# Optimization experiments

Hardware: AMD Instinct MI355X
Metric: run time of the kernel (lower is better)

## Reference

```python
import jax, jax.numpy as jnp
import numpy as np

N_NODES = 50000
N_EDGES = 800000
D_IN = 64
D_HID = 64
N_LAYERS = 3
BN_EPS = 1e-5


def setup_inputs() -> dict:
    key = jax.random.key(0)
    ks = jax.random.split(key, 10)
    x = jax.random.normal(ks[0], (N_NODES, D_IN), dtype=jnp.float32)
    edge_index = jax.random.randint(ks[1], (2, N_EDGES), 0, N_NODES, dtype=jnp.int32)
    # Per-layer GCN weights (in==hid==64 so we can stack) and BatchNorm params.
    Ws = jax.random.normal(ks[2], (N_LAYERS, D_HID, D_HID), dtype=jnp.float32) / np.sqrt(D_HID)
    bs = jnp.zeros((N_LAYERS, D_HID), dtype=jnp.float32)
    gammas = jnp.ones((N_LAYERS, D_HID), dtype=jnp.float32)
    betas = jnp.zeros((N_LAYERS, D_HID), dtype=jnp.float32)
    means = jax.random.normal(ks[3], (N_LAYERS, D_HID), dtype=jnp.float32) * 0.1
    variances = jax.random.uniform(ks[4], (N_LAYERS, D_HID), dtype=jnp.float32, minval=0.5, maxval=1.5)
    lin_w = jax.random.normal(ks[5], (D_HID, 1), dtype=jnp.float32) / np.sqrt(D_HID)
    lin_b = jnp.zeros((1,), dtype=jnp.float32)
    return {"x": x, "edge_index": edge_index, "Ws": Ws, "bs": bs,
            "gammas": gammas, "betas": betas, "means": means,
            "variances": variances, "lin_w": lin_w, "lin_b": lin_b}


def _gnn_forward(x, edge_index, Ws, bs, gammas, betas, means, variances, lin_w, lin_b):
    n = x.shape[0]
    # GCNConv: add self loops, symmetric D^{-1/2}(A+I)D^{-1/2} normalization.
    loop = jnp.arange(n, dtype=edge_index.dtype)
    row = jnp.concatenate([edge_index[0], loop])  # source nodes
    col = jnp.concatenate([edge_index[1], loop])  # target nodes
    deg = jax.ops.segment_sum(jnp.ones(row.shape[0], x.dtype), col, num_segments=n)
    dinv = jax.lax.rsqrt(jnp.maximum(deg, 1.0))  # deg >= 1 from self loops
    norm = (dinv[row] * dinv[col])[:, None]  # [E+N, 1]

    h = x
    for i in range(N_LAYERS):
        h = h @ Ws[i]  # transform first (PyG GCNConv order)
        h = jax.ops.segment_sum(h[row] * norm, col, num_segments=n) + bs[i]
        # BatchNorm1d (eval mode: running stats) + ReLU; dropout is identity in eval.
        h = (h - means[i]) * jax.lax.rsqrt(variances[i] + BN_EPS) * gammas[i] + betas[i]
        h = jax.nn.relu(h)
    out = h @ lin_w + lin_b  # [N, 1]
    return out[:, 0]


def reference(x, edge_index, Ws, bs, gammas, betas, means, variances, lin_w, lin_b):
    return _gnn_forward(x, edge_index, Ws, bs, gammas, betas, means, variances, lin_w, lin_b)
```

## Files before the change

### kernel.cpp

```cpp
#include <hip/hip_runtime.h>
#include <hip/hip_bf16.h>


#define BN_EPS 1e-5f
#define CAP 64
#define CHUNK 4096
#define SEGCAP 5120
#define NBINS_MAX 256

__global__ __launch_bounds__(256) void k_bin_pairs(const int* __restrict__ row,
                                                   const int* __restrict__ col,
                                                   int* __restrict__ gfill,
                                                   unsigned int* __restrict__ gpairs,
                                                   int e, int nbins) {
    __shared__ unsigned int pl[CHUNK];
    __shared__ int bcnt[NBINS_MAX];
    __shared__ int bbase[NBINS_MAX];
    int tid = threadIdx.x;
    int base = blockIdx.x * CHUNK;
    for (int b = tid; b < nbins; b += 256) bcnt[b] = 0;
    __syncthreads();
    int nloc = e - base; if (nloc > CHUNK) nloc = CHUNK;
    #pragma unroll
    for (int it = 0; it < CHUNK / 1024; ++it) {
        int le = (it * 256 + tid) * 4;
        if (le + 3 < nloc) {
            int i4 = (base >> 2) + it * 256 + tid;
            int4 r = ((const int4*)row)[i4];
            int4 c = ((const int4*)col)[i4];
            atomicAdd(&bcnt[c.x >> 8], 1); pl[le + 0] = (unsigned)r.x | ((unsigned)c.x << 16);
            atomicAdd(&bcnt[c.y >> 8], 1); pl[le + 1] = (unsigned)r.y | ((unsigned)c.y << 16);
            atomicAdd(&bcnt[c.z >> 8], 1); pl[le + 2] = (unsigned)r.z | ((unsigned)c.z << 16);
            atomicAdd(&bcnt[c.w >> 8], 1); pl[le + 3] = (unsigned)r.w | ((unsigned)c.w << 16);
        } else {
            for (int j = 0; j < 4; ++j) {
                if (le + j < nloc) {
                    int rr = row[base + le + j];
                    int cc = col[base + le + j];
                    atomicAdd(&bcnt[cc >> 8], 1);
                    pl[le + j] = (unsigned)rr | ((unsigned)cc << 16);
                }
            }
        }
    }
    __syncthreads();
    for (int b = tid; b < nbins; b += 256) {
        bbase[b] = atomicAdd(&gfill[b], bcnt[b]);
        bcnt[b] = 0;
    }
    __syncthreads();
    for (int i = tid; i < nloc; i += 256) {
        unsigned int p = pl[i];
        int bin = p >> 24;
        int off = atomicAdd(&bcnt[bin], 1);
        int pos = bbase[bin] + off;
        if (pos < SEGCAP) gpairs[(size_t)bin * SEGCAP + pos] = p;
    }
}

__global__ __launch_bounds__(256) void k_bucket_build(const unsigned int* __restrict__ gpairs,
                                                      const int* __restrict__ gfill,
                                                      int* __restrict__ cnt,
                                                      unsigned short* __restrict__ bucket,
                                                      int n) {
    __shared__ unsigned short lb[256 * CAP];
    __shared__ int lc[256];
    int tid = threadIdx.x;
    int bin = blockIdx.x;
    lc[tid] = 0;
    __syncthreads();
    int m = gfill[bin]; if (m > SEGCAP) m = SEGCAP;
    const unsigned int* seg = gpairs + (size_t)bin * SEGCAP;
    for (int i = tid; i < m; i += 256) {
        unsigned int p = seg[i];
        int src = p & 0xffff;
        int dl = (p >> 16) & 255;
        int pos = atomicAdd(&lc[dl], 1);
        if (pos < CAP) lb[dl * CAP + pos] = (unsigned short)src;
    }
    __syncthreads();
    int nodebase = bin << 8;
    const int4* lb4 = (const int4*)lb;
    int4* gb4 = (int4*)bucket;
    for (int i = tid; i < 256 * 8; i += 256) {
        int rrow = i >> 3;
        int gnode = nodebase + rrow;
        if (gnode < n) gb4[(size_t)gnode * 8 + (i & 7)] = lb4[i];
    }
    int gnode = nodebase + tid;
    if (gnode < n) cnt[gnode] = lc[tid];
}

template<int LAYER>
__global__ __launch_bounds__(256) void k_matmul(const float* __restrict__ A,
                                                const float* __restrict__ W,
                                                const int* __restrict__ cnt,
                                                float* __restrict__ out, int n) {
    __shared__ float hs[64 * 65];
    __shared__ float wsh[64 * 64];
    int tid = threadIdx.x;
    int rbase = blockIdx.x * 64;
    for (int i = tid; i < 4096; i += 256) wsh[i] = W[i];
    for (int i = tid; i < 4096; i += 256) {
        int r = i >> 6, c = i & 63;
        int gr = rbase + r;
        hs[r * 65 + c] = (gr < n) ? A[gr * 64 + c] : 0.f;
    }
    __syncthreads();
    int r = tid & 63;
    int cg = tid >> 6;
    float4 a0 = {0, 0, 0, 0}, a1 = a0, a2 = a0, a3 = a0;
    const float4* W4 = (const float4*)wsh;
    #pragma unroll 8
    for (int k = 0; k < 64; ++k) {
        float hv = hs[r * 65 + k];
        float4 w0 = W4[k * 16 + cg * 4 + 0];
        float4 w1 = W4[k * 16 + cg * 4 + 1];
        float4 w2 = W4[k * 16 + cg * 4 + 2];
        float4 w3 = W4[k * 16 + cg * 4 + 3];
        a0.x = fmaf(hv, w0.x, a0.x); a0.y = fmaf(hv, w0.y, a0.y);
        a0.z = fmaf(hv, w0.z, a0.z); a0.w = fmaf(hv, w0.w, a0.w);
        a1.x = fmaf(hv, w1.x, a1.x); a1.y = fmaf(hv, w1.y, a1.y);
        a1.z = fmaf(hv, w1.z, a1.z); a1.w = fmaf(hv, w1.w, a1.w);
        a2.x = fmaf(hv, w2.x, a2.x); a2.y = fmaf(hv, w2.y, a2.y);
        a2.z = fmaf(hv, w2.z, a2.z); a2.w = fmaf(hv, w2.w, a2.w);
        a3.x = fmaf(hv, w3.x, a3.x); a3.y = fmaf(hv, w3.y, a3.y);
        a3.z = fmaf(hv, w3.z, a3.z); a3.w = fmaf(hv, w3.w, a3.w);
    }
    int gr = rbase + r;
    if (gr < n) {
        float d = rsqrtf((float)(cnt[gr] + 1));
        a0.x *= d; a0.y *= d; a0.z *= d; a0.w *= d;
        a1.x *= d; a1.y *= d; a1.z *= d; a1.w *= d;
        a2.x *= d; a2.y *= d; a2.z *= d; a2.w *= d;
        a3.x *= d; a3.y *= d; a3.z *= d; a3.w *= d;
        float4* o = (float4*)(out + gr * 64 + cg * 16);
        o[0] = a0; o[1] = a1; o[2] = a2; o[3] = a3;
    }
}

template<int LAYER, bool FINAL>
__global__ __launch_bounds__(256) void k_agg(const float* __restrict__ t,
                                             const int* __restrict__ cnt,
                                             const unsigned short* __restrict__ bucket,
                                             const float* __restrict__ bias,
                                             const float* __restrict__ gamma,
                                             const float* __restrict__ beta,
                                             const float* __restrict__ mean,
                                             const float* __restrict__ var,
                                             float* __restrict__ hout,
                                             const float* __restrict__ lw,
                                             const float* __restrict__ lb,
                                             float* __restrict__ outp, int n) {
    int node = (blockIdx.x * blockDim.x + threadIdx.x) >> 6;
    if (node >= n) return;
    int lane = threadIdx.x & 63;
    int g = lane >> 4;
    int fl = (lane & 15) << 2;
    int c = cnt[node];
    int myidx = (int)bucket[node * CAP + lane];
    float4 acc = {0.f, 0.f, 0.f, 0.f};
    int sub = 0;
    for (; sub + 8 <= c; sub += 8) {
        int sA = __shfl(myidx, sub + g, 64);
        int sB = __shfl(myidx, sub + 4 + g, 64);
        float4 vA = *(const float4*)(t + (size_t)sA * 64 + fl);
        float4 vB = *(const float4*)(t + (size_t)sB * 64 + fl);
        acc.x += vA.x; acc.y += vA.y; acc.z += vA.z; acc.w += vA.w;
        acc.x += vB.x; acc.y += vB.y; acc.z += vB.z; acc.w += vB.w;
    }
    for (; sub < c; sub += 4) {
        int j = sub + g;
        int jj = (j < c) ? j : c - 1;
        int sA = __shfl(myidx, jj, 64);
        if (j < c) {
            float4 v = *(const float4*)(t + (size_t)sA * 64 + fl);
            acc.x += v.x; acc.y += v.y; acc.z += v.z; acc.w += v.w;
        }
    }
    acc.x += __shfl_down(acc.x, 32, 64); acc.y += __shfl_down(acc.y, 32, 64);
    acc.z += __shfl_down(acc.z, 32, 64); acc.w += __shfl_down(acc.w, 32, 64);
    acc.x += __shfl_down(acc.x, 16, 64); acc.y += __shfl_down(acc.y, 16, 64);
    acc.z += __shfl_down(acc.z, 16, 64); acc.w += __shfl_down(acc.w, 16, 64);
    if (lane < 16) {
        float di = rsqrtf((float)(c + 1));
        float4 self = *(const float4*)(t + (size_t)node * 64 + fl);
        float4 b4 = *(const float4*)(bias + fl);
        float4 m4 = *(const float4*)(mean + fl);
        float4 v4 = *(const float4*)(var + fl);
        float4 g4 = *(const float4*)(gamma + fl);
        float4 be4 = *(const float4*)(beta + fl);
        float4 r;
        r.x = fmaf(acc.x + self.x, di, b4.x);
        r.y = fmaf(acc.y + self.y, di, b4.y);
        r.z = fmaf(acc.z + self.z, di, b4.z);
        r.w = fmaf(acc.w + self.w, di, b4.w);
        float4 h;
        h.x = fmaxf(fmaf(r.x - m4.x, g4.x * rsqrtf(v4.x + BN_EPS), be4.x), 0.f);
        h.y = fmaxf(fmaf(r.y - m4.y, g4.y * rsqrtf(v4.y + BN_EPS), be4.y), 0.f);
        h.z = fmaxf(fmaf(r.z - m4.z, g4.z * rsqrtf(v4.z + BN_EPS), be4.z), 0.f);
        h.w = fmaxf(fmaf(r.w - m4.w, g4.w * rsqrtf(v4.w + BN_EPS), be4.w), 0.f);
        if (FINAL) {
            float4 w4 = *(const float4*)(lw + fl);
            float p = h.x * w4.x + h.y * w4.y + h.z * w4.z + h.w * w4.w;
            p += __shfl_down(p, 8, 64);
            p += __shfl_down(p, 4, 64);
            p += __shfl_down(p, 2, 64);
            p += __shfl_down(p, 1, 64);
            if (lane == 0) outp[node] = p + lb[0];
        } else {
            *(float4*)(hout + (size_t)node * 64 + fl) = h;
        }
    }
}

extern "C" void kernel_launch(void* const* d_in, const int* in_sizes, int n_in,
                              void* d_out, int out_size, void* d_ws, size_t ws_size,
                              hipStream_t stream) {
    const float* x    = (const float*)d_in[0];
    const int*   ei   = (const int*)d_in[1];
    const float* Ws   = (const float*)d_in[2];
    const float* bs   = (const float*)d_in[3];
    const float* gam  = (const float*)d_in[4];
    const float* bet  = (const float*)d_in[5];
    const float* mean = (const float*)d_in[6];
    const float* var  = (const float*)d_in[7];
    const float* lw   = (const float*)d_in[8];
    const float* lb   = (const float*)d_in[9];
    float* out = (float*)d_out;

    const int n = in_sizes[0] / 64;
    const int e = in_sizes[1] / 2;
    const int* row = ei;
    const int* col = ei + e;
    const int nbins = (n + 255) >> 8;

    int*   ws_i = (int*)d_ws;
    float* ws_f = (float*)d_ws;
    int* cnt = ws_i;
    int* gfill = ws_i + n;
    unsigned short* bucket = (unsigned short*)(ws_i + n + 256);
    float* tbuf = ws_f + n + 256 + 32 * (size_t)n;
    float* hbuf = tbuf + 64 * (size_t)n;
    unsigned int* gpairs = (unsigned int*)tbuf;

    int nb_p1 = (e + CHUNK - 1) / CHUNK;
    int nb_w = (n + 3) / 4;
    int nb_mm = (n + 63) / 64;

    hipMemsetAsync(gfill, 0, 256 * sizeof(int), stream);
    k_bin_pairs<<<nb_p1, 256, 0, stream>>>(row, col, gfill, gpairs, e, nbins);
    k_bucket_build<<<nbins, 256, 0, stream>>>(gpairs, gfill, cnt, bucket, n);

    k_matmul<0><<<nb_mm, 256, 0, stream>>>(x, Ws + 0 * 4096, cnt, tbuf, n);
    k_agg<0, false><<<nb_w, 256, 0, stream>>>(tbuf, cnt, bucket,
                                              bs, gam, bet, mean, var,
                                              hbuf, nullptr, nullptr, nullptr, n);
    k_matmul<1><<<nb_mm, 256, 0, stream>>>(hbuf, Ws + 1 * 4096, cnt, tbuf, n);
    k_agg<1, false><<<nb_w, 256, 0, stream>>>(tbuf, cnt, bucket,
                                              bs + 64, gam + 64, bet + 64, mean + 64, var + 64,
                                              hbuf, nullptr, nullptr, nullptr, n);
    k_matmul<2><<<nb_mm, 256, 0, stream>>>(hbuf, Ws + 2 * 4096, cnt, tbuf, n);
    k_agg<2, true><<<nb_w, 256, 0, stream>>>(tbuf, cnt, bucket,
                                             bs + 128, gam + 128, bet + 128, mean + 128, var + 128,
                                             nullptr, lw, lb, out, n);
}
```

Baseline: 271.5 us.

## Fuse GCN matmul into aggregation by reordering aggregate-then-transform per layer

Uses linearity to aggregate first and multiply by W afterwards. This folds the separate matmul kernels into a single persistent per-layer kernel that keeps W columns in registers and does the 64x64 transform through wave shuffles. The input is pre-scaled by the degree normalisation once, and each layer writes its output already scaled for the next. The goal is to cut three kernel launches and a full read/write round trip of the feature matrix per layer. The cost is 64 shuffle-FMA steps per node, heavy register use from the 64-float array, and a grid fixed at 1024 blocks.

```diff
diff --git a/kernel.cpp b/kernel.cpp
--- a/kernel.cpp
+++ b/kernel.cpp
@@ -91,125 +91,102 @@
     if (gnode < n) cnt[gnode] = lc[tid];
 }
 
-template<int LAYER>
-__global__ __launch_bounds__(256) void k_matmul(const float* __restrict__ A,
-                                                const float* __restrict__ W,
-                                                const int* __restrict__ cnt,
-                                                float* __restrict__ out, int n) {
-    __shared__ float hs[64 * 65];
-    __shared__ float wsh[64 * 64];
-    int tid = threadIdx.x;
-    int rbase = blockIdx.x * 64;
-    for (int i = tid; i < 4096; i += 256) wsh[i] = W[i];
-    for (int i = tid; i < 4096; i += 256) {
-        int r = i >> 6, c = i & 63;
-        int gr = rbase + r;
-        hs[r * 65 + c] = (gr < n) ? A[gr * 64 + c] : 0.f;
-    }
-    __syncthreads();
-    int r = tid & 63;
-    int cg = tid >> 6;
-    float4 a0 = {0, 0, 0, 0}, a1 = a0, a2 = a0, a3 = a0;
-    const float4* W4 = (const float4*)wsh;
-    #pragma unroll 8
-    for (int k = 0; k < 64; ++k) {
-        float hv = hs[r * 65 + k];
-        float4 w0 = W4[k * 16 + cg * 4 + 0];
-        float4 w1 = W4[k * 16 + cg * 4 + 1];
-        float4 w2 = W4[k * 16 + cg * 4 + 2];
-        float4 w3 = W4[k * 16 + cg * 4 + 3];
-        a0.x = fmaf(hv, w0.x, a0.x); a0.y = fmaf(hv, w0.y, a0.y);
-        a0.z = fmaf(hv, w0.z, a0.z); a0.w = fmaf(hv, w0.w, a0.w);
-        a1.x = fmaf(hv, w1.x, a1.x); a1.y = fmaf(hv, w1.y, a1.y);
-        a1.z = fmaf(hv, w1.z, a1.z); a1.w = fmaf(hv, w1.w, a1.w);
-        a2.x = fmaf(hv, w2.x, a2.x); a2.y = fmaf(hv, w2.y, a2.y);
-        a2.z = fmaf(hv, w2.z, a2.z); a2.w = fmaf(hv, w2.w, a2.w);
-        a3.x = fmaf(hv, w3.x, a3.x); a3.y = fmaf(hv, w3.y, a3.y);
-        a3.z = fmaf(hv, w3.z, a3.z); a3.w = fmaf(hv, w3.w, a3.w);
-    }
-    int gr = rbase + r;
-    if (gr < n) {
-        float d = rsqrtf((float)(cnt[gr] + 1));
-        a0.x *= d; a0.y *= d; a0.z *= d; a0.w *= d;
-        a1.x *= d; a1.y *= d; a1.z *= d; a1.w *= d;
-        a2.x *= d; a2.y *= d; a2.z *= d; a2.w *= d;
-        a3.x *= d; a3.y *= d; a3.z *= d; a3.w *= d;
-        float4* o = (float4*)(out + gr * 64 + cg * 16);
-        o[0] = a0; o[1] = a1; o[2] = a2; o[3] = a3;
+__global__ __launch_bounds__(256) void k_prescale(const float* __restrict__ x,
+                                                  const int* __restrict__ cnt,
+                                                  float* __restrict__ t, int n16) {
+    int i = blockIdx.x * blockDim.x + threadIdx.x;
+    if (i < n16) {
+        int node = i >> 4;
+        float d = rsqrtf((float)(cnt[node] + 1));
+        float4 v = ((const float4*)x)[i];
+        v.x *= d; v.y *= d; v.z *= d; v.w *= d;
+        ((float4*)t)[i] = v;
     }
 }
 
 template<int LAYER, bool FINAL>
-__global__ __launch_bounds__(256) void k_agg(const float* __restrict__ t,
-                                             const int* __restrict__ cnt,
-                                             const unsigned short* __restrict__ bucket,
-                                             const float* __restrict__ bias,
-                                             const float* __restrict__ gamma,
-                                             const float* __restrict__ beta,
-                                             const float* __restrict__ mean,
-                                             const float* __restrict__ var,
-                                             float* __restrict__ hout,
-                                             const float* __restrict__ lw,
-                                             const float* __restrict__ lb,
-                                             float* __restrict__ outp, int n) {
-    int node = (blockIdx.x * blockDim.x + threadIdx.x) >> 6;
-    if (node >= n) return;
+__global__ __launch_bounds__(256, 4) void k_layer(const float* __restrict__ t,
+                                                  const int* __restrict__ cnt,
+                                                  const unsigned short* __restrict__ bucket,
+                                                  const float* __restrict__ W,
+                                                  const float* __restrict__ bias,
+                                                  const float* __restrict__ gamma,
+                                                  const float* __restrict__ beta,
+                                                  const float* __restrict__ mean,
+                                                  const float* __restrict__ var,
+                                                  float* __restrict__ hout,
+                                                  const float* __restrict__ lw,
+                                                  const float* __restrict__ lb,
+                                                  float* __restrict__ outp, int n) {
     int lane = threadIdx.x & 63;
+    float wreg[64];
+    #pragma unroll
+    for (int k = 0; k < 64; ++k) wreg[k] = W[k * 64 + lane];
+    float bn_b  = bias[lane];
+    float bn_m  = mean[lane];
+    float bn_s  = gamma[lane] * rsqrtf(var[lane] + BN_EPS);
+    float bn_be = beta[lane];
+    float lwv   = FINAL ? lw[lane] : 0.f;
     int g = lane >> 4;
     int fl = (lane & 15) << 2;
-    int c = cnt[node];
-    int myidx = (int)bucket[node * CAP + lane];
-    float4 acc = {0.f, 0.f, 0.f, 0.f};
-    int sub = 0;
-    for (; sub + 8 <= c; sub += 8) {
-        int sA = __shfl(myidx, sub + g, 64);
-        int sB = __shfl(myidx, sub + 4 + g, 64);
-        float4 vA = *(const float4*)(t + (size_t)sA * 64 + fl);
-        float4 vB = *(const float4*)(t + (size_t)sB * 64 + fl);
-        acc.x += vA.x; acc.y += vA.y; acc.z += vA.z; acc.w += vA.w;
-        acc.x += vB.x; acc.y += vB.y; acc.z += vB.z; acc.w += vB.w;
-    }
-    for (; sub < c; sub += 4) {
-        int j = sub + g;
-        int jj = (j < c) ? j : c - 1;
-        int sA = __shfl(myidx, jj, 64);
-        if (j < c) {
-            float4 v = *(const float4*)(t + (size_t)sA * 64 + fl);
-            acc.x += v.x; acc.y += v.y; acc.z += v.z; acc.w += v.w;
-        }
-    }
-    acc.x += __shfl_down(acc.x, 32, 64); acc.y += __shfl_down(acc.y, 32, 64);
-    acc.z += __shfl_down(acc.z, 32, 64); acc.w += __shfl_down(acc.w, 32, 64);
-    acc.x += __shfl_down(acc.x, 16, 64); acc.y += __shfl_down(acc.y, 16, 64);
-    acc.z += __shfl_down(acc.z, 16, 64); acc.w += __shfl_down(acc.w, 16, 64);
-    if (lane < 16) {
+    int wave = (blockIdx.x * blockDim.x + threadIdx.x) >> 6;
+    int nwaves = (gridDim.x * blockDim.x) >> 6;
+    for (int node = wave; node < n; node += nwaves) {
+        int c = cnt[node];
+        int myidx = (int)bucket[node * CAP + lane];
+        float4 acc = {0.f, 0.f, 0.f, 0.f};
+        int sub = 0;
+        for (; sub + 8 <= c; sub += 8) {
+            int sA = __shfl(myidx, sub + g, 64);
+            int sB = __shfl(myidx, sub + 4 + g, 64);
+            float4 vA = *(const float4*)(t + (size_t)sA * 64 + fl);
+            float4 vB = *(const float4*)(t + (size_t)sB * 64 + fl);
+            acc.x += vA.x; acc.y += vA.y; acc.z += vA.z; acc.w += vA.w;
+            acc.x += vB.x; acc.y += vB.y; acc.z += vB.z; acc.w += vB.w;
+        }
+        for (; sub < c; sub += 4) {
+            int j = sub + g;
+            int jj = (j < c) ? j : c - 1;
+            int sA = __shfl(myidx, jj, 64);
+            if (j < c) {
+                float4 v = *(const float4*)(t + (size_t)sA * 64 + fl);
+                acc.x += v.x; acc.y += v.y; acc.z += v.z; acc.w += v.w;
+            }
+        }
+        acc.x += __shfl_down(acc.x, 32, 64); acc.y += __shfl_down(acc.y, 32, 64);
+        acc.z += __shfl_down(acc.z, 32, 64); acc.w += __shfl_down(acc.w, 32, 64);
+        acc.x += __shfl_down(acc.x, 16, 64); acc.y += __shfl_down(acc.y, 16, 64);
+        acc.z += __shfl_down(acc.z, 16, 64); acc.w += __shfl_down(acc.w, 16, 64);
+        if (lane < 16) {
+            float4 self = *(const float4*)(t + (size_t)node * 64 + fl);
+            acc.x += self.x; acc.y += self.y; acc.z += self.z; acc.w += self.w;
+        }
+        float y = 0.f;
+        #pragma unroll
+        for (int q = 0; q < 16; ++q) {
+            float ax = __shfl(acc.x, q, 64);
+            float ay = __shfl(acc.y, q, 64);
+            float az = __shfl(acc.z, q, 64);
+            float aw = __shfl(acc.w, q, 64);
+            y = fmaf(ax, wreg[4 * q + 0], y);
+            y = fmaf(ay, wreg[4 * q + 1], y);
+            y = fmaf(az, wreg[4 * q + 2], y);
+            y = fmaf(aw, wreg[4 * q + 3], y);
+        }
         float di = rsqrtf((float)(c + 1));
-        float4 self = *(const float4*)(t + (size_t)node * 64 + fl);
-        float4 b4 = *(const float4*)(bias + fl);
-        float4 m4 = *(const float4*)(mean + fl);
-        float4 v4 = *(const float4*)(var + fl);
-        float4 g4 = *(const float4*)(gamma + fl);
-        float4 be4 = *(const float4*)(beta + fl);
-        float4 r;
-        r.x = fmaf(acc.x + self.x, di, b4.x);
-        r.y = fmaf(acc.y + self.y, di, b4.y);
-        r.z = fmaf(acc.z + self.z, di, b4.z);
-        r.w = fmaf(acc.w + self.w, di, b4.w);
-        float4 h;
-        h.x = fmaxf(fmaf(r.x - m4.x, g4.x * rsqrtf(v4.x + BN_EPS), be4.x), 0.f);
-        h.y = fmaxf(fmaf(r.y - m4.y, g4.y * rsqrtf(v4.y + BN_EPS), be4.y), 0.f);
-        h.z = fmaxf(fmaf(r.z - m4.z, g4.z * rsqrtf(v4.z + BN_EPS), be4.z), 0.f);
-        h.w = fmaxf(fmaf(r.w - m4.w, g4.w * rsqrtf(v4.w + BN_EPS), be4.w), 0.f);
+        float z = fmaf(y, di, bn_b);
+        float h = fmaxf(fmaf(z - bn_m, bn_s, bn_be), 0.f);
         if (FINAL) {
-            float4 w4 = *(const float4*)(lw + fl);
-            float p = h.x * w4.x + h.y * w4.y + h.z * w4.z + h.w * w4.w;
+            float p = h * lwv;
+            p += __shfl_down(p, 32, 64);
+            p += __shfl_down(p, 16, 64);
             p += __shfl_down(p, 8, 64);
             p += __shfl_down(p, 4, 64);
             p += __shfl_down(p, 2, 64);
             p += __shfl_down(p, 1, 64);
             if (lane == 0) outp[node] = p + lb[0];
         } else {
-            *(float4*)(hout + (size_t)node * 64 + fl) = h;
+            hout[(size_t)node * 64 + lane] = h * di;
         }
     }
 }
@@ -245,23 +222,22 @@
     unsigned int* gpairs = (unsigned int*)tbuf;
 
     int nb_p1 = (e + CHUNK - 1) / CHUNK;
-    int nb_w = (n + 3) / 4;
-    int nb_mm = (n + 63) / 64;
+    int n16 = n * 16;
+    int nb_ps = (n16 + 255) / 256;
+    int nb_ly = 1024;
 
     hipMemsetAsync(gfill, 0, 256 * sizeof(int), stream);
     k_bin_pairs<<<nb_p1, 256, 0, stream>>>(row, col, gfill, gpairs, e, nbins);
     k_bucket_build<<<nbins, 256, 0, stream>>>(gpairs, gfill, cnt, bucket, n);
-
-    k_matmul<0><<<nb_mm, 256, 0, stream>>>(x, Ws + 0 * 4096, cnt, tbuf, n);
-    k_agg<0, false><<<nb_w, 256, 0, stream>>>(tbuf, cnt, bucket,
-                                              bs, gam, bet, mean, var,
-                                              hbuf, nullptr, nullptr, nullptr, n);
-    k_matmul<1><<<nb_mm, 256, 0, stream>>>(hbuf, Ws + 1 * 4096, cnt, tbuf, n);
-    k_agg<1, false><<<nb_w, 256, 0, stream>>>(tbuf, cnt, bucket,
-                                              bs + 64, gam + 64, bet + 64, mean + 64, var + 64,
-                                              hbuf, nullptr, nullptr, nullptr, n);
-    k_matmul<2><<<nb_mm, 256, 0, stream>>>(hbuf, Ws + 2 * 4096, cnt, tbuf, n);
-    k_agg<2, true><<<nb_w, 256, 0, stream>>>(tbuf, cnt, bucket,
-                                             bs + 128, gam + 128, bet + 128, mean + 128, var + 128,
-                                             nullptr, lw, lb, out, n);
-}
+    k_prescale<<<nb_ps, 256, 0, stream>>>(x, cnt, tbuf, n16);
+
+    k_layer<0, false><<<nb_ly, 256, 0, stream>>>(tbuf, cnt, bucket, Ws,
+                                                 bs, gam, bet, mean, var,
+                                                 hbuf, nullptr, nullptr, nullptr, n);
+    k_layer<1, false><<<nb_ly, 256, 0, stream>>>(hbuf, cnt, bucket, Ws + 4096,
+                                                 bs + 64, gam + 64, bet + 64, mean + 64, var + 64,
+                                                 tbuf, nullptr, nullptr, nullptr, n);
+    k_layer<2, true><<<nb_ly, 256, 0, stream>>>(tbuf, cnt, bucket, Ws + 8192,
+                                                bs + 128, gam + 128, bet + 128, mean + 128, var + 128,
+                                                nullptr, lw, lb, out, n);
+}
```

Result: faster. 264.3 us (-2.7%).
